# Kernel optimization log

Hardware: AMD Instinct MI355X
Metric: run time of the kernel (lower is better)

Reference implementation:

```python
import jax, jax.numpy as jnp
import numpy as np
from jax import lax

G = 8        # group_num
BS = 32      # blocksize
SC = 13      # sample_channel = round(32*32*0.1/8)


def conv2d(x, w, b=None, stride=1, pad=0):
    y = lax.conv_general_dilated(x, w, (stride, stride), [(pad, pad), (pad, pad)],
                                 dimension_numbers=("NCHW", "OIHW", "NCHW"))
    if b is not None:
        y = y + b[None, :, None, None]
    return y


def prelu(x, a):
    return jnp.where(x >= 0, x, a * x)


def depth_to_space(x, bs):
    # matches Reshape_Concat_Adap: channel index = c_out*bs*bs + i*bs + j
    b, c, h, w = x.shape
    co = c // (bs * bs)
    x = x.reshape(b, co, bs, bs, h, w)
    x = x.transpose(0, 1, 4, 2, 5, 3)  # b, co, h, bs, w, bs
    return x.reshape(b, co, h * bs, w * bs)


def setup_inputs() -> dict:
    key = jax.random.key(0)
    ks = jax.random.split(key, 16)
    s = 0.05
    inp = {
        "x": jax.random.normal(ks[0], (8, 1, 256, 256), jnp.float32),
        "sample_w": jax.random.normal(ks[1], (G, SC, 1, BS, BS), jnp.float32) * 0.02,
        "up_w": jax.random.normal(ks[2], (G, BS * BS, SC, 1, 1), jnp.float32) * s,
        "up_b": jnp.zeros((G, BS * BS), jnp.float32),
        "conv1_w": jax.random.normal(ks[3], (G, 64, 1, 3, 3), jnp.float32) * s,
        "conv1_b": jnp.zeros((G, 64), jnp.float32),
        "conv1_a": jnp.full((G,), 0.25, jnp.float32),
        "fus_w": jax.random.normal(ks[4], (G - 1, 64, 128, 3, 3), jnp.float32) * s,
        "fus_b": jnp.zeros((G - 1, 64), jnp.float32),
        "fus_a": jnp.full((G - 1,), 0.25, jnp.float32),
        "t2_w": jax.random.normal(ks[5], (G, 64, 64, 3, 3), jnp.float32) * s,
        "t2_b": jnp.zeros((G, 64), jnp.float32),
        "t2_a": jnp.full((G,), 0.25, jnp.float32),
        "t3_w": jax.random.normal(ks[6], (G, 64, 64, 3, 3), jnp.float32) * s,
        "t3_b": jnp.zeros((G, 64), jnp.float32),
        "t3_a": jnp.full((G,), 0.25, jnp.float32),
        "t4_w": jax.random.normal(ks[7], (G, 64, 64, 3, 3), jnp.float32) * s,
        "t4_b": jnp.zeros((G, 64), jnp.float32),
        "t4_a": jnp.full((G,), 0.25, jnp.float32),
        "t5_w": jax.random.normal(ks[8], (G, 1, 64, 3, 3), jnp.float32) * s,
        "t5_b": jnp.zeros((G, 1), jnp.float32),
    }
    return inp


def reference(x, sample_w, up_w, up_b, conv1_w, conv1_b, conv1_a,
              fus_w, fus_b, fus_a, t2_w, t2_b, t2_a, t3_w, t3_b, t3_a,
              t4_w, t4_b, t4_a, t5_w, t5_b):
    def head(g):
        y = conv2d(x, sample_w[g], stride=BS)              # [B,SC,H/32,W/32]
        y = conv2d(y, up_w[g], up_b[g])                    # [B,1024,H/32,W/32]
        y = depth_to_space(y, BS)                          # [B,1,H,W]
        return prelu(conv2d(y, conv1_w[g], conv1_b[g], pad=1), conv1_a[g])

    def tail(h, g):
        h = prelu(conv2d(h, t2_w[g], t2_b[g], pad=1), t2_a[g])
        h = prelu(conv2d(h, t3_w[g], t3_b[g], pad=1), t3_a[g])
        h = prelu(conv2d(h, t4_w[g], t4_b[g], pad=1), t4_a[g])
        return conv2d(h, t5_w[g], t5_b[g], pad=1)          # [B,1,H,W]

    heads = [head(g) for g in range(G)]
    cur = heads[0]
    outs = [tail(cur, 0)]
    for m in range(G - 1):
        cat = jnp.concatenate([cur, heads[m + 1]], axis=1)  # [B,128,H,W]
        cur = prelu(conv2d(cat, fus_w[m], fus_b[m], pad=1), fus_a[m])
        outs.append(tail(cur, m + 1))
    return jnp.stack(outs, axis=0)  # [G,B,1,H,W]
```

## Files before the change

kernel.cpp:

```cpp
#include <hip/hip_runtime.h>
#include <stdint.h>

typedef __attribute__((ext_vector_type(8))) short short8;
typedef __attribute__((ext_vector_type(16))) float floatx16;

#define PLANE16 8388608

__device__ __forceinline__ float b2f(short s) {
  union { uint32_t u; float f; } v; v.u = ((uint32_t)(uint16_t)s) << 16; return v.f;
}
__device__ __forceinline__ short f2b(float f) {
  union { float f; uint32_t u; } v; v.f = f;
  uint32_t r = (v.u + 0x7FFFu + ((v.u >> 16) & 1u)) >> 16;
  return (short)r;
}

__device__ __forceinline__ uint32_t ldsA(int r, int xp, int c) {
  uint32_t byte = ((uint32_t)(r * 258 + xp) << 5) + ((uint32_t)c << 1);
  byte ^= (uint32_t)((((xp >> 2) ^ (xp >> 3) ^ (xp >> 4)) & 1) << 4);
  return byte;
}

template<int NC16>
__global__ __launch_bounds__(512, 2)
void k_conv(const short* __restrict__ in1, const short* __restrict__ in2,
            const short* __restrict__ wp, const float* __restrict__ bias,
            const float* __restrict__ alpha, short* __restrict__ out)
{
  __shared__ __align__(16) uint8_t smem[3 * 258 * 32];
  const int wg = blockIdx.x;
  const int b = wg & 7;
  const int y = wg >> 3;
  const int tid = threadIdx.x;
  const int l = tid & 63;
  const int w = tid >> 6;
  const int lm = l & 31;
  const int lh = l >> 5;

  floatx16 acc[2];
  #pragma unroll
  for (int nb = 0; nb < 2; ++nb)
    #pragma unroll
    for (int r = 0; r < 16; ++r) acc[nb][r] = 0.f;

  const int xbase = w * 32 + lm;

  short8 stg[3];

  auto issue = [&](int c16) {
    const short* __restrict__ src =
        ((c16 < 4) ? in1 : in2) + (size_t)(c16 & 3) * PLANE16;
    #pragma unroll
    for (int i = 0; i < 3; ++i) {
      int widx = tid + i * 512;
      int r = widx >> 9;
      int rem = widx & 511;
      int xp = (rem >> 1) + 1;
      int half = rem & 1;
      int yy = y + r - 1;
      short8 v = {0, 0, 0, 0, 0, 0, 0, 0};
      if ((unsigned)yy < 256u)
        v = *(const short8*)(src + ((b * 256 + yy) * 256 + (xp - 1)) * 16 + half * 8);
      stg[i] = v;
    }
  };
  auto commit = [&]() {
    #pragma unroll
    for (int i = 0; i < 3; ++i) {
      int widx = tid + i * 512;
      int r = widx >> 9;
      int rem = widx & 511;
      int xp = (rem >> 1) + 1;
      int half = rem & 1;
      *(short8*)(smem + ldsA(r, xp, half * 8)) = stg[i];
    }
  };

  if (tid < 12) {
    short8 z = {0, 0, 0, 0, 0, 0, 0, 0};
    int r = tid >> 2;
    int xp = (tid & 2) ? 257 : 0;
    int half = tid & 1;
    *(short8*)(smem + ldsA(r, xp, half * 8)) = z;
  }

  issue(0);
  commit();
  __syncthreads();

  #pragma unroll
  for (int c16 = 0; c16 < NC16; ++c16) {
    if (c16 + 1 < NC16) issue(c16 + 1);

    __builtin_amdgcn_s_setprio(1);
    #pragma unroll
    for (int ky = 0; ky < 3; ++ky)
    #pragma unroll
    for (int kx = 0; kx < 3; ++kx) {
      const int ks = c16 * 9 + ky * 3 + kx;
      const short8 bw0 = *(const short8*)(wp + ((ks * 2 + 0) * 64 + l) * 8);
      const short8 bw1 = *(const short8*)(wp + ((ks * 2 + 1) * 64 + l) * 8);
      const int cl = lh * 8;
      const int xp = xbase + kx;
      const short8 av = *(const short8*)(smem + ldsA(ky, xp, cl));
      acc[0] = __builtin_amdgcn_mfma_f32_32x32x16_bf16(av, bw0, acc[0], 0, 0, 0);
      acc[1] = __builtin_amdgcn_mfma_f32_32x32x16_bf16(av, bw1, acc[1], 0, 0, 0);
    }
    __builtin_amdgcn_s_setprio(0);

    if (c16 + 1 < NC16) {
      __syncthreads();
      commit();
      __syncthreads();
    }
  }

  const float alp = alpha[0];
  #pragma unroll
  for (int nb = 0; nb < 2; ++nb) {
    const float bs = bias[nb * 32 + lm];
    short* __restrict__ op = out + (size_t)(nb * 2 + (lm >> 4)) * PLANE16 + (lm & 15);
    #pragma unroll
    for (int r = 0; r < 16; ++r) {
      int px = w * 32 + (r & 3) + ((r >> 2) << 3) + (lh << 2);
      float v = acc[nb][r] + bs;
      v = v >= 0.f ? v : alp * v;
      op[((b * 256 + y) * 256 + px) * 16] = f2b(v);
    }
  }
}

__global__ __launch_bounds__(256)
void k_pack(const float* __restrict__ w2, const float* __restrict__ w3,
            const float* __restrict__ w4, const float* __restrict__ wf,
            short* __restrict__ wp234, short* __restrict__ wpfus)
{
  int idx = blockIdx.x * 256 + threadIdx.x;
  if (idx < 24 * 36864) {
    int conv = idx / 36864;
    int r = idx - conv * 36864;
    int which = conv >> 3, g = conv & 7;
    const float* W = (which == 0 ? w2 : which == 1 ? w3 : w4) + g * 36864;
    int ks = r >> 10;
    int nblk = (r >> 9) & 1;
    int lane = (r >> 3) & 63;
    int e = r & 7;
    int c16 = ks / 9;
    int t = ks - c16 * 9;
    int cin = c16 * 16 + ((lane >> 5) << 3) + e;
    int cout = nblk * 32 + (lane & 31);
    int ky = t / 3, kx = t % 3;
    wp234[idx] = f2b(W[((cout * 64 + cin) * 3 + ky) * 3 + kx]);
  } else {
    int idx2 = idx - 24 * 36864;
    if (idx2 >= 7 * 73728) return;
    int conv = idx2 / 73728;
    int r = idx2 - conv * 73728;
    const float* W = wf + conv * 73728;
    int ks = r >> 10;
    int nblk = (r >> 9) & 1;
    int lane = (r >> 3) & 63;
    int e = r & 7;
    int c16 = ks / 9;
    int t = ks - c16 * 9;
    int cin = c16 * 16 + ((lane >> 5) << 3) + e;
    int cout = nblk * 32 + (lane & 31);
    int ky = t / 3, kx = t % 3;
    wpfus[idx2] = f2b(W[((cout * 128 + cin) * 3 + ky) * 3 + kx]);
  }
}

__global__ __launch_bounds__(256)
void k_sample(const float* __restrict__ x, const float* __restrict__ sw,
              float* __restrict__ s_all)
{
  int idx = blockIdx.x * 256 + threadIdx.x;
  int gx = idx & 7, gy = (idx >> 3) & 7;
  int t = idx >> 6;
  int c = t % 13; t /= 13;
  int b = t & 7, g = t >> 3;
  const float* xb = x + b * 65536 + (gy * 32) * 256 + gx * 32;
  const float* wp = sw + (g * 13 + c) * 1024;
  float acc = 0.f;
  for (int i = 0; i < 32; ++i) {
    #pragma unroll
    for (int j = 0; j < 32; ++j) acc += xb[i * 256 + j] * wp[i * 32 + j];
  }
  s_all[idx] = acc;
}

__global__ __launch_bounds__(256)
void k_upz(const float* __restrict__ s_all, const float* __restrict__ upw,
           const float* __restrict__ upb, float* __restrict__ z_all)
{
  int idx = blockIdx.x * 256 + threadIdx.x;
  int x = idx & 255, y = (idx >> 8) & 255;
  int b = (idx >> 16) & 7, g = idx >> 19;
  int pos = (y & 31) * 32 + (x & 31);
  int gy = y >> 5, gx = x >> 5;
  const float* sp = s_all + ((g * 8 + b) * 13) * 64 + gy * 8 + gx;
  const float* wp = upw + (g * 1024 + pos) * 13;
  float a = upb[g * 1024 + pos];
  #pragma unroll
  for (int c = 0; c < 13; ++c) a += wp[c] * sp[c * 64];
  z_all[idx] = a;
}

__global__ __launch_bounds__(256)
void k_conv1(const float* __restrict__ z, const float* __restrict__ w,
             const float* __restrict__ bias, const float* __restrict__ alpha,
             short* __restrict__ out)
{
  int wg = blockIdx.x;
  int b = wg & 7;
  int y = wg >> 3;
  int x = threadIdx.x;
  int pid = (b * 256 + y) * 256 + x;
  float zv[9];
  #pragma unroll
  for (int t = 0; t < 9; ++t) {
    int dy = t / 3, dx = t % 3;
    int yy = y + dy - 1, xx = x + dx - 1;
    zv[t] = ((unsigned)yy < 256u && (unsigned)xx < 256u)
              ? z[b * 65536 + yy * 256 + xx] : 0.f;
  }
  float alp = alpha[0];
  #pragma unroll
  for (int c0 = 0; c0 < 64; c0 += 8) {
    short8 pack;
    #pragma unroll
    for (int e = 0; e < 8; ++e) {
      int c = c0 + e;
      float a = bias[c];
      #pragma unroll
      for (int t = 0; t < 9; ++t) a += w[c * 9 + t] * zv[t];
      a = a >= 0.f ? a : alp * a;
      pack[e] = f2b(a);
    }
    *(short8*)(out + (size_t)(c0 >> 4) * PLANE16 + pid * 16 + (c0 & 8)) = pack;
  }
}

__global__ __launch_bounds__(256)
void k_t5(const short* __restrict__ in, const float* __restrict__ w,
          const float* __restrict__ bias, float* __restrict__ out)
{
  int wg = blockIdx.x;
  int b = wg & 7;
  int y = wg >> 3;
  int x = threadIdx.x;
  float acc = bias[0];
  for (int dy = 0; dy < 3; ++dy) {
    int yy = y + dy - 1;
    if ((unsigned)yy >= 256u) continue;
    for (int dx = 0; dx < 3; ++dx) {
      int xx = x + dx - 1;
      if ((unsigned)xx >= 256u) continue;
      const int pix = (b * 256 + yy) * 256 + xx;
      #pragma unroll
      for (int c0 = 0; c0 < 64; c0 += 8) {
        short8 v = *(const short8*)(in + (size_t)(c0 >> 4) * PLANE16 + pix * 16 + (c0 & 8));
        #pragma unroll
        for (int e = 0; e < 8; ++e)
          acc += w[(c0 + e) * 9 + dy * 3 + dx] * b2f(v[e]);
      }
    }
  }
  out[(b * 256 + y) * 256 + x] = acc;
}

extern "C" void kernel_launch(void* const* d_in, const int* in_sizes, int n_in,
                              void* d_out, int out_size, void* d_ws, size_t ws_size,
                              hipStream_t stream) {
  const float* X   = (const float*)d_in[0];
  const float* SW  = (const float*)d_in[1];
  const float* UPW = (const float*)d_in[2];
  const float* UPB = (const float*)d_in[3];
  const float* C1W = (const float*)d_in[4];
  const float* C1B = (const float*)d_in[5];
  const float* C1A = (const float*)d_in[6];
  const float* FW  = (const float*)d_in[7];
  const float* FB  = (const float*)d_in[8];
  const float* FA  = (const float*)d_in[9];
  const float* W2  = (const float*)d_in[10];
  const float* B2  = (const float*)d_in[11];
  const float* A2  = (const float*)d_in[12];
  const float* W3  = (const float*)d_in[13];
  const float* B3  = (const float*)d_in[14];
  const float* A3  = (const float*)d_in[15];
  const float* W4  = (const float*)d_in[16];
  const float* B4  = (const float*)d_in[17];
  const float* A4  = (const float*)d_in[18];
  const float* W5  = (const float*)d_in[19];
  const float* B5  = (const float*)d_in[20];
  float* OUT = (float*)d_out;
  (void)in_sizes; (void)n_in; (void)out_size; (void)ws_size;

  uint8_t* base = (uint8_t*)d_ws;
  size_t off = 0;
  auto alloc = [&](size_t bytes) -> uint8_t* {
    uint8_t* r = base + off;
    off += (bytes + 255) & ~(size_t)255;
    return r;
  };
  const size_t ACT_ELEMS = 4ull * PLANE16;
  short* act[3];
  for (int i = 0; i < 3; ++i) act[i] = (short*)alloc(ACT_ELEMS * 2);
  float* z_all = (float*)alloc(4194304ull * 4);
  float* s_all = (float*)alloc(53248ull * 4);
  short* wp234 = (short*)alloc(884736ull * 2);
  short* wpfus = (short*)alloc(516096ull * 2);

  k_pack<<<dim3(5472), dim3(256), 0, stream>>>(W2, W3, W4, FW, wp234, wpfus);
  k_sample<<<dim3(208), dim3(256), 0, stream>>>(X, SW, s_all);
  k_upz<<<dim3(16384), dim3(256), 0, stream>>>(s_all, UPW, UPB, z_all);

  int cur = 0, A = 1, B = 2;
  k_conv1<<<dim3(2048), dim3(256), 0, stream>>>(z_all, C1W, C1B, C1A, act[cur]);

  for (int m = 0; m < 8; ++m) {
    const short* wp_t2 = wp234 + (0 * 8 + m) * 36864;
    const short* wp_t3 = wp234 + (1 * 8 + m) * 36864;
    const short* wp_t4 = wp234 + (2 * 8 + m) * 36864;

    k_conv<4><<<dim3(2048), dim3(512), 0, stream>>>(
        act[cur], act[cur], wp_t2, B2 + m * 64, A2 + m, act[A]);
    k_conv<4><<<dim3(2048), dim3(512), 0, stream>>>(
        act[A], act[A], wp_t3, B3 + m * 64, A3 + m, act[B]);
    k_conv<4><<<dim3(2048), dim3(512), 0, stream>>>(
        act[B], act[B], wp_t4, B4 + m * 64, A4 + m, act[A]);
    k_t5<<<dim3(2048), dim3(256), 0, stream>>>(
        act[A], W5 + m * 576, B5 + m, OUT + (size_t)m * 524288);

    if (m < 7) {
      k_conv1<<<dim3(2048), dim3(256), 0, stream>>>(
          z_all + (size_t)(m + 1) * 524288, C1W + (m + 1) * 576,
          C1B + (m + 1) * 64, C1A + (m + 1), act[B]);
      k_conv<8><<<dim3(2048), dim3(512), 0, stream>>>(
          act[cur], act[B], wpfus + m * 73728, FB + m * 64, FA + m, act[A]);
      int tmp = cur; cur = A; A = tmp;
    }
  }
}
```

Baseline: 2.666 ms.

## Load conv input operands directly from global memory instead of LDS staging

Removes the shared-memory staging buffer, the register double-buffering of the next channel chunk, and the barriers around it. Each MFMA A-operand is now read straight from global memory with per-lane bounds checks for the padding. This drops the LDS writes and syncs but relies on L1/L2 to serve the ninefold reuse of each input row across the 3x3 taps, and it loses the overlap between loading the next chunk and computing the current one.

```diff
diff --git a/kernel.cpp b/kernel.cpp
--- a/kernel.cpp
+++ b/kernel.cpp
@@ -13,12 +13,6 @@
   union { float f; uint32_t u; } v; v.f = f;
   uint32_t r = (v.u + 0x7FFFu + ((v.u >> 16) & 1u)) >> 16;
   return (short)r;
-}
-
-__device__ __forceinline__ uint32_t ldsA(int r, int xp, int c) {
-  uint32_t byte = ((uint32_t)(r * 258 + xp) << 5) + ((uint32_t)c << 1);
-  byte ^= (uint32_t)((((xp >> 2) ^ (xp >> 3) ^ (xp >> 4)) & 1) << 4);
-  return byte;
 }
 
 template<int NC16>
@@ -27,7 +21,6 @@
             const short* __restrict__ wp, const float* __restrict__ bias,
             const float* __restrict__ alpha, short* __restrict__ out)
 {
-  __shared__ __align__(16) uint8_t smem[3 * 258 * 32];
   const int wg = blockIdx.x;
   const int b = wg & 7;
   const int y = wg >> 3;
@@ -43,75 +36,27 @@
     #pragma unroll
     for (int r = 0; r < 16; ++r) acc[nb][r] = 0.f;
 
-  const int xbase = w * 32 + lm;
-
-  short8 stg[3];
-
-  auto issue = [&](int c16) {
+  #pragma unroll
+  for (int c16 = 0; c16 < NC16; ++c16) {
     const short* __restrict__ src =
         ((c16 < 4) ? in1 : in2) + (size_t)(c16 & 3) * PLANE16;
-    #pragma unroll
-    for (int i = 0; i < 3; ++i) {
-      int widx = tid + i * 512;
-      int r = widx >> 9;
-      int rem = widx & 511;
-      int xp = (rem >> 1) + 1;
-      int half = rem & 1;
-      int yy = y + r - 1;
-      short8 v = {0, 0, 0, 0, 0, 0, 0, 0};
-      if ((unsigned)yy < 256u)
-        v = *(const short8*)(src + ((b * 256 + yy) * 256 + (xp - 1)) * 16 + half * 8);
-      stg[i] = v;
-    }
-  };
-  auto commit = [&]() {
-    #pragma unroll
-    for (int i = 0; i < 3; ++i) {
-      int widx = tid + i * 512;
-      int r = widx >> 9;
-      int rem = widx & 511;
-      int xp = (rem >> 1) + 1;
-      int half = rem & 1;
-      *(short8*)(smem + ldsA(r, xp, half * 8)) = stg[i];
-    }
-  };
-
-  if (tid < 12) {
-    short8 z = {0, 0, 0, 0, 0, 0, 0, 0};
-    int r = tid >> 2;
-    int xp = (tid & 2) ? 257 : 0;
-    int half = tid & 1;
-    *(short8*)(smem + ldsA(r, xp, half * 8)) = z;
-  }
-
-  issue(0);
-  commit();
-  __syncthreads();
-
-  #pragma unroll
-  for (int c16 = 0; c16 < NC16; ++c16) {
-    if (c16 + 1 < NC16) issue(c16 + 1);
-
-    __builtin_amdgcn_s_setprio(1);
-    #pragma unroll
-    for (int ky = 0; ky < 3; ++ky)
-    #pragma unroll
-    for (int kx = 0; kx < 3; ++kx) {
-      const int ks = c16 * 9 + ky * 3 + kx;
-      const short8 bw0 = *(const short8*)(wp + ((ks * 2 + 0) * 64 + l) * 8);
-      const short8 bw1 = *(const short8*)(wp + ((ks * 2 + 1) * 64 + l) * 8);
-      const int cl = lh * 8;
-      const int xp = xbase + kx;
-      const short8 av = *(const short8*)(smem + ldsA(ky, xp, cl));
-      acc[0] = __builtin_amdgcn_mfma_f32_32x32x16_bf16(av, bw0, acc[0], 0, 0, 0);
-      acc[1] = __builtin_amdgcn_mfma_f32_32x32x16_bf16(av, bw1, acc[1], 0, 0, 0);
-    }
-    __builtin_amdgcn_s_setprio(0);
-
-    if (c16 + 1 < NC16) {
-      __syncthreads();
-      commit();
-      __syncthreads();
+
+    #pragma unroll
+    for (int ky = 0; ky < 3; ++ky) {
+      const int yy = y + ky - 1;
+      const bool rowok = (unsigned)yy < 256u;
+      #pragma unroll
+      for (int kx = 0; kx < 3; ++kx) {
+        const int ks = c16 * 9 + ky * 3 + kx;
+        const short8 bw0 = *(const short8*)(wp + ((ks * 2 + 0) * 64 + l) * 8);
+        const short8 bw1 = *(const short8*)(wp + ((ks * 2 + 1) * 64 + l) * 8);
+        const int xx = w * 32 + lm + kx - 1;
+        short8 av = {0, 0, 0, 0, 0, 0, 0, 0};
+        if (rowok && (unsigned)xx < 256u)
+          av = *(const short8*)(src + ((b * 256 + yy) * 256 + xx) * 16 + lh * 8);
+        acc[0] = __builtin_amdgcn_mfma_f32_32x32x16_bf16(av, bw0, acc[0], 0, 0, 0);
+        acc[1] = __builtin_amdgcn_mfma_f32_32x32x16_bf16(av, bw1, acc[1], 0, 0, 0);
+      }
     }
   }
 
```

Result: slower. 2.827 ms (+6.1%).
